# Performance work log

Hardware: AMD Instinct MI355X
Metric: run time of the kernel (lower is better)

Reference implementation:

```python
import jax, jax.numpy as jnp
import numpy as np

B, T, D, H = 8, 2048, 1024, 128  # batch, seq (== context_length), d_model, head_size


def setup_inputs() -> dict:
    key = jax.random.key(0)
    kx, kq, kk, kv = jax.random.split(key, 4)
    scale = 0.02
    return {
        "x": jax.random.normal(kx, (B, T, D), dtype=jnp.float32),
        "Wq": jax.random.normal(kq, (D, H), dtype=jnp.float32) * scale,
        "Wk": jax.random.normal(kk, (D, H), dtype=jnp.float32) * scale,
        "Wv": jax.random.normal(kv, (D, H), dtype=jnp.float32) * scale,
    }


def reference(x, Wq, Wk, Wv):
    # bias-free linear projections (torch nn.Linear(bias=False))
    q = jnp.einsum("btd,dh->bth", x, Wq)
    k = jnp.einsum("btd,dh->bth", x, Wk)
    v = jnp.einsum("btd,dh->bth", x, Wv)
    head_size = q.shape[-1]
    # scores: [B, T, T], scaled by 1/sqrt(head_size)
    scores = jnp.einsum("bqh,bkh->bqk", q, k) * (1.0 / jnp.sqrt(jnp.float32(head_size)))
    # causal mask (tril): positions k > q get -inf before softmax
    t = scores.shape[-1]
    causal = jnp.tril(jnp.ones((t, t), dtype=bool))
    scores = jnp.where(causal, scores, -jnp.inf)
    weights = jax.nn.softmax(scores, axis=-1)
    # dropout is identity in eval mode (deterministic reference)
    return jnp.einsum("bqk,bkh->bqh", weights, v)
```

## Files before the change

kernel.cpp:

```cpp
#include <hip/hip_runtime.h>
#include <hip/hip_bf16.h>
#include <stdint.h>

typedef __bf16 bf16x8 __attribute__((ext_vector_type(8)));
typedef float f32x4 __attribute__((ext_vector_type(4)));
typedef unsigned short u16;
typedef u16 u16x8 __attribute__((ext_vector_type(8)));

#define GAS __attribute__((address_space(1)))
#define LAS __attribute__((address_space(3)))

static constexpr int Tn = 2048;
static constexpr int Dn = 1024;
static constexpr int Hn = 128;

__device__ __forceinline__ u16 bf16u(float f) {
  __bf16 h = (__bf16)f;
  return __builtin_bit_cast(u16, h);
}
__device__ __forceinline__ float u16f(u16 u) {
  uint32_t t = (uint32_t)u << 16;
  return __builtin_bit_cast(float, t);
}

__device__ __forceinline__ void gl_lds16(const void* g, void* l) {
  __builtin_amdgcn_global_load_lds((GAS void*)g, (LAS void*)l, 16, 0, 0);
}

__global__ __launch_bounds__(256) void convert_w_kernel(
    const float* __restrict__ Wq, const float* __restrict__ Wk,
    const float* __restrict__ Wv, u16* __restrict__ WT) {
  const int bid = blockIdx.x;
  const int w = bid >> 7;
  const int h = bid & 127;
  const float* src = (w == 0) ? Wq : ((w == 1) ? Wk : Wv);
  const float scale = (w == 0) ? 0.08838834764831845f : 1.0f;
  const int d0 = threadIdx.x * 4;
  ushort4 v;
  v.x = bf16u(src[(size_t)(d0 + 0) * Hn + h] * scale);
  v.y = bf16u(src[(size_t)(d0 + 1) * Hn + h] * scale);
  v.z = bf16u(src[(size_t)(d0 + 2) * Hn + h] * scale);
  v.w = bf16u(src[(size_t)(d0 + 3) * Hn + h] * scale);
  *(ushort4*)(&WT[(size_t)(w * Hn + h) * Dn + d0]) = v;
}

__global__ __launch_bounds__(512, 4) void qkv_gemm_kernel(
    const float* __restrict__ x, const u16* __restrict__ WT,
    u16* __restrict__ qb, u16* __restrict__ kb, u16* __restrict__ vb) {
  __shared__ u16 As[32 * 64];
  __shared__ u16 Bs[384 * 64];
  const int m0 = blockIdx.x * 32;
  const int tid = threadIdx.x;
  const int lane = tid & 63;
  const int wid = tid >> 6;
  const int l15 = lane & 15;
  const int g = lane >> 4;
  const int g4 = g * 4;

  const f32x4 fz = {0.f, 0.f, 0.f, 0.f};
  f32x4 acc[2][3];
#pragma unroll
  for (int i = 0; i < 2; ++i)
#pragma unroll
    for (int j = 0; j < 3; ++j) acc[i][j] = fz;

  const int arow = tid >> 4;
  const int c16 = tid & 15;
  const int aslot = (c16 >> 1) ^ (arow & 7);
  const int ahalf = c16 & 1;
  const float* aptr = x + (size_t)(m0 + arow) * Dn + c16 * 4;

  float4 fa = *(const float4*)(aptr);

  for (int k0 = 0; k0 < Dn; k0 += 64) {
    {
      ushort4 pk;
      pk.x = bf16u(fa.x); pk.y = bf16u(fa.y); pk.z = bf16u(fa.z); pk.w = bf16u(fa.w);
      *(ushort4*)(&As[arow * 64 + aslot * 8 + ahalf * 4]) = pk;
    }
#pragma unroll
    for (int i = 0; i < 6; ++i) {
      const int s = i * 512 + tid;
      const int n = s >> 3;
      const int us = s & 7;
      const u16* gsrc = WT + (size_t)n * Dn + k0 + ((us ^ (n & 7)) * 8);
      gl_lds16(gsrc, &Bs[(i * 512 + wid * 64) * 8]);
    }
    __syncthreads();
    {
      const int k1 = (k0 + 64 < Dn) ? k0 + 64 : k0;
      fa = *(const float4*)(aptr + k1);
    }
#pragma unroll
    for (int kc = 0; kc < 2; ++kc) {
      bf16x8 af[2], bfr[3];
#pragma unroll
      for (int mi = 0; mi < 2; ++mi) {
        const int row = mi * 16 + l15;
        af[mi] = *(const bf16x8*)(&As[row * 64 + (((kc * 4 + g) ^ (row & 7)) * 8)]);
      }
#pragma unroll
      for (int ni = 0; ni < 3; ++ni) {
        const int n = wid * 48 + ni * 16 + l15;
        bfr[ni] = *(const bf16x8*)(&Bs[n * 64 + (((kc * 4 + g) ^ (n & 7)) * 8)]);
      }
#pragma unroll
      for (int mi = 0; mi < 2; ++mi)
#pragma unroll
        for (int ni = 0; ni < 3; ++ni)
          acc[mi][ni] = __builtin_amdgcn_mfma_f32_16x16x32_bf16(af[mi], bfr[ni], acc[mi][ni], 0, 0, 0);
    }
    __builtin_amdgcn_s_barrier();
  }
#pragma unroll
  for (int mi = 0; mi < 2; ++mi)
#pragma unroll
    for (int ni = 0; ni < 3; ++ni) {
      const int nb = wid * 48 + ni * 16;
      const int w = nb >> 7;
      u16* dst = (w == 0) ? qb : ((w == 1) ? kb : vb);
      const int h = (nb & 127) + l15;
#pragma unroll
      for (int r = 0; r < 4; ++r)
        dst[(size_t)(m0 + mi * 16 + g4 + r) * Hn + h] = bf16u(acc[mi][ni][r]);
    }
}

__global__ __launch_bounds__(256) void transpose_v_kernel(
    const u16* __restrict__ vb, u16* __restrict__ vt) {
  __shared__ u16 tile[64 * 64];
  const int bid = blockIdx.x;
  const int b = bid >> 6;
  const int rem = bid & 63;
  const int t0 = (rem >> 1) * 64, h0 = (rem & 1) * 64;
  const int tid = threadIdx.x;
  {
    const int r = tid >> 2, cq = tid & 3;
    const u16* src = vb + (size_t)(b * Tn + t0 + r) * Hn + h0 + cq * 16;
#pragma unroll
    for (int s = 0; s < 2; ++s) {
      u16x8 v = *(const u16x8*)(src + s * 8);
      const int u = cq * 2 + s;
      *(u16x8*)(&tile[r * 64 + (u ^ (r & 7)) * 8]) = v;
    }
  }
  __syncthreads();
  {
    const int hr = tid >> 2, tg = tid & 3;
    u16 outv[16];
#pragma unroll
    for (int j = 0; j < 16; ++j) {
      const int tl = tg * 16 + j;
      outv[j] = tile[tl * 64 + (((hr >> 3) ^ (tl & 7)) * 8) + (hr & 7)];
    }
    u16* dstp = vt + (size_t)(b * Hn + h0 + hr) * Tn + t0 + tg * 16;
    *(u16x8*)(dstp) = *(const u16x8*)(&outv[0]);
    *(u16x8*)(dstp + 8) = *(const u16x8*)(&outv[8]);
  }
}

__global__ __launch_bounds__(256, 2) void attention_kernel(
    const u16* __restrict__ qb, const u16* __restrict__ kb,
    const u16* __restrict__ vt, u16* __restrict__ po,
    float* __restrict__ pm, float* __restrict__ pl) {
  __shared__ u16 Ks[2][64 * 128];
  __shared__ u16 Vs[2][128 * 64];
  __shared__ u16 Pb[4][16 * 64];

  const int bid = blockIdx.x;
  const int b = bid & 7;
  const int rest = bid >> 3;
  const int s = rest & 1;
  const int kk = rest >> 1;
  const int qblk = (kk & 1) ? (kk >> 1) : (31 - (kk >> 1));
  const int qb0 = qblk * 64;

  const int tid = threadIdx.x;
  const int wid = tid >> 6;
  const int lane = tid & 63;
  const int l15 = lane & 15;
  const int g = lane >> 4;
  const int g4 = g * 4;
  const int t0w = qb0 + wid * 16;

  const u16* qB = qb + (size_t)b * Tn * Hn;
  const u16* kB = kb + (size_t)b * Tn * Hn;
  const u16* vB = vt + (size_t)b * Hn * Tn;

  bf16x8 qf[4];
#pragma unroll
  for (int kc = 0; kc < 4; ++kc)
    qf[kc] = *(const bf16x8*)(qB + (size_t)(t0w + l15) * Hn + kc * 32 + g * 8);

  const f32x4 fz = {0.f, 0.f, 0.f, 0.f};
  f32x4 o[8];
#pragma unroll
  for (int hc = 0; hc < 8; ++hc) o[hc] = fz;
  float m[4], lsum[4];
#pragma unroll
  for (int r = 0; r < 4; ++r) { m[r] = -__builtin_inff(); lsum[r] = 0.f; }

  u16* P = &Pb[wid][0];
  const int ntiles = (qblk >= s) ? ((qblk - s) >> 1) + 1 : 0;

  auto stage = [&](int buf, int kv0) {
#pragma unroll
    for (int j = 0; j < 4; ++j) {
      const int U = j * 256 + tid;
      const int row = U >> 4, us = U & 15;
      const u16* gsrc = kB + (size_t)(kv0 + row) * Hn + ((us ^ (row & 15)) * 8);
      gl_lds16(gsrc, &Ks[buf][(j * 256 + wid * 64) * 8]);
    }
#pragma unroll
    for (int j = 0; j < 4; ++j) {
      const int U = j * 256 + tid;
      const int h = U >> 3, us = U & 7;
      const u16* gsrc = vB + (size_t)h * Tn + kv0 + ((us ^ (h & 7)) * 8);
      gl_lds16(gsrc, &Vs[buf][(j * 256 + wid * 64) * 8]);
    }
  };

  if (ntiles > 0) {
    stage(0, s * 64);
    __syncthreads();
    for (int i = 0; i < ntiles; ++i) {
      const int cur = i & 1;
      if (i + 1 < ntiles) stage(cur ^ 1, (s + 2 * (i + 1)) * 64);
      const int kv0 = (s + 2 * i) * 64;
      const u16* Kl = &Ks[cur][0];
      const u16* Vl = &Vs[cur][0];

      f32x4 S[4];
#pragma unroll
      for (int cn = 0; cn < 4; ++cn) S[cn] = fz;
#pragma unroll
      for (int cn = 0; cn < 4; ++cn) {
#pragma unroll
        for (int kc = 0; kc < 4; ++kc) {
          const int row = cn * 16 + l15;
          const int unit = (kc * 4 + g) ^ (row & 15);
          const bf16x8 kf = *(const bf16x8*)(&Kl[row * 128 + unit * 8]);
          S[cn] = __builtin_amdgcn_mfma_f32_16x16x32_bf16(qf[kc], kf, S[cn], 0, 0, 0);
        }
      }
      if (kv0 + 63 > t0w) {
#pragma unroll
        for (int cn = 0; cn < 4; ++cn) {
          const int kv = kv0 + cn * 16 + l15;
#pragma unroll
          for (int r = 0; r < 4; ++r)
            if (kv > t0w + g4 + r) S[cn][r] = -__builtin_inff();
        }
      }
      float mloc[4];
#pragma unroll
      for (int r = 0; r < 4; ++r)
        mloc[r] = fmaxf(fmaxf(S[0][r], S[1][r]), fmaxf(S[2][r], S[3][r]));
#pragma unroll
      for (int st = 1; st <= 8; st <<= 1)
#pragma unroll
        for (int r = 0; r < 4; ++r)
          mloc[r] = fmaxf(mloc[r], __shfl_xor(mloc[r], st, 64));
      float sc[4], mnew[4];
#pragma unroll
      for (int r = 0; r < 4; ++r) {
        mnew[r] = fmaxf(m[r], mloc[r]);
        sc[r] = __expf(m[r] - mnew[r]);
        m[r] = mnew[r];
      }
      float psum[4] = {0.f, 0.f, 0.f, 0.f};
#pragma unroll
      for (int cn = 0; cn < 4; ++cn)
#pragma unroll
        for (int r = 0; r < 4; ++r) {
          const float p = __expf(S[cn][r] - mnew[r]);
          S[cn][r] = p;
          psum[r] += p;
        }
#pragma unroll
      for (int st = 1; st <= 8; st <<= 1)
#pragma unroll
        for (int r = 0; r < 4; ++r) psum[r] += __shfl_xor(psum[r], st, 64);
#pragma unroll
      for (int r = 0; r < 4; ++r) lsum[r] = lsum[r] * sc[r] + psum[r];
#pragma unroll
      for (int hc = 0; hc < 8; ++hc)
#pragma unroll
        for (int r = 0; r < 4; ++r) o[hc][r] *= sc[r];
      asm volatile("s_waitcnt lgkmcnt(0)" ::: "memory");
#pragma unroll
      for (int cn = 0; cn < 4; ++cn)
#pragma unroll
        for (int r = 0; r < 4; ++r) {
          const int q = g4 + r;
          const int col = cn * 16 + l15;
          P[q * 64 + (col ^ ((q & 7) << 3))] = bf16u(S[cn][r]);
        }
      asm volatile("s_waitcnt lgkmcnt(0)" ::: "memory");
      bf16x8 pf[2];
#pragma unroll
      for (int kvc = 0; kvc < 2; ++kvc)
        pf[kvc] = *(const bf16x8*)(&P[l15 * 64 + (((kvc * 32 + g * 8) ^ ((l15 & 7) << 3)))]);
#pragma unroll
      for (int hc = 0; hc < 8; ++hc) {
#pragma unroll
        for (int kvc = 0; kvc < 2; ++kvc) {
          const int h = hc * 16 + l15;
          const int unit = (kvc * 4 + g) ^ (h & 7);
          const bf16x8 vf = *(const bf16x8*)(&Vl[h * 64 + unit * 8]);
          o[hc] = __builtin_amdgcn_mfma_f32_16x16x32_bf16(pf[kvc], vf, o[hc], 0, 0, 0);
        }
      }
      __syncthreads();
    }
  }

  u16* poS = po + ((size_t)(s * 8 + b) * Tn + t0w) * Hn;
#pragma unroll
  for (int hc = 0; hc < 8; ++hc)
#pragma unroll
    for (int r = 0; r < 4; ++r)
      poS[(size_t)(g4 + r) * Hn + hc * 16 + l15] = bf16u(o[hc][r]);
  if (l15 == 0) {
#pragma unroll
    for (int r = 0; r < 4; ++r) {
      pm[(size_t)(s * 8 + b) * Tn + t0w + g4 + r] = m[r];
      pl[(size_t)(s * 8 + b) * Tn + t0w + g4 + r] = lsum[r];
    }
  }
}

__global__ __launch_bounds__(256) void merge_kernel(
    const u16* __restrict__ po, const float* __restrict__ pm,
    const float* __restrict__ pl, float* __restrict__ out) {
  const int tid = threadIdx.x;
  const int row = blockIdx.x * 8 + (tid >> 5);
  const int h0 = (tid & 31) * 4;
  const float m0 = pm[row], m1 = pm[8 * Tn + row];
  const float l0 = pl[row], l1 = pl[8 * Tn + row];
  const float M = fmaxf(m0, m1);
  const float e0 = __expf(m0 - M), e1 = __expf(m1 - M);
  const float invL = 1.0f / (e0 * l0 + e1 * l1);
  const ushort4 a = *(const ushort4*)(po + (size_t)row * Hn + h0);
  const ushort4 c = *(const ushort4*)(po + (size_t)(8 * Tn + row) * Hn + h0);
  float4 r;
  r.x = (e0 * u16f(a.x) + e1 * u16f(c.x)) * invL;
  r.y = (e0 * u16f(a.y) + e1 * u16f(c.y)) * invL;
  r.z = (e0 * u16f(a.z) + e1 * u16f(c.z)) * invL;
  r.w = (e0 * u16f(a.w) + e1 * u16f(c.w)) * invL;
  *(float4*)(out + (size_t)row * Hn + h0) = r;
}

extern "C" void kernel_launch(void* const* d_in, const int* in_sizes, int n_in,
                              void* d_out, int out_size, void* d_ws, size_t ws_size,
                              hipStream_t stream) {
  const float* x  = (const float*)d_in[0];
  const float* Wq = (const float*)d_in[1];
  const float* Wk = (const float*)d_in[2];
  const float* Wv = (const float*)d_in[3];
  float* out = (float*)d_out;
  char* ws = (char*)d_ws;
  u16* WT = (u16*)(ws);
  u16* qb = (u16*)(ws + (1u << 20));
  u16* kb = (u16*)(ws + (5u << 20));
  u16* vb = (u16*)(ws + (9u << 20));
  u16* vt = (u16*)(ws + (13u << 20));
  u16* po = (u16*)(ws + (17u << 20));
  float* pm = (float*)(ws + (25u << 20));
  float* pl = (float*)(ws + (25u << 20) + (1u << 18));

  convert_w_kernel<<<384, 256, 0, stream>>>(Wq, Wk, Wv, WT);
  qkv_gemm_kernel<<<512, 512, 0, stream>>>(x, WT, qb, kb, vb);
  transpose_v_kernel<<<512, 256, 0, stream>>>(vb, vt);
  attention_kernel<<<512, 256, 0, stream>>>(qb, kb, vt, po, pm, pl);
  merge_kernel<<<2048, 256, 0, stream>>>(po, pm, pl, out);
}
```

Measured before the change: 165.4 us.

## Fuse V transpose into QKV GEMM epilogue and double-buffer with larger M tile

The QKV projection kernel now processes 64 rows per block instead of 32, double-buffers its A and B shared-memory tiles so the next k-slice loads while the current one computes, and writes V directly in transposed layout. This removes the separate transpose kernel launch and the extra round-trip of V through global memory, and it halves redundant re-reads of the weight matrix. In exchange it doubles LDS use per block, lowers the occupancy hint from 4 to 2, and launches only 256 blocks. The transposed V stores are 4-element ushort4 writes strided by T.

```diff
diff --git a/kernel.cpp b/kernel.cpp
--- a/kernel.cpp
+++ b/kernel.cpp
@@ -44,12 +44,12 @@
   *(ushort4*)(&WT[(size_t)(w * Hn + h) * Dn + d0]) = v;
 }
 
-__global__ __launch_bounds__(512, 4) void qkv_gemm_kernel(
+__global__ __launch_bounds__(512, 2) void qkv_gemm_kernel(
     const float* __restrict__ x, const u16* __restrict__ WT,
-    u16* __restrict__ qb, u16* __restrict__ kb, u16* __restrict__ vb) {
-  __shared__ u16 As[32 * 64];
-  __shared__ u16 Bs[384 * 64];
-  const int m0 = blockIdx.x * 32;
+    u16* __restrict__ qb, u16* __restrict__ kb, u16* __restrict__ vt) {
+  __shared__ u16 As[2][64 * 64];
+  __shared__ u16 Bs[2][384 * 64];
+  const int m0 = blockIdx.x * 64;
   const int tid = threadIdx.x;
   const int lane = tid & 63;
   const int wid = tid >> 6;
@@ -58,105 +58,98 @@
   const int g4 = g * 4;
 
   const f32x4 fz = {0.f, 0.f, 0.f, 0.f};
-  f32x4 acc[2][3];
-#pragma unroll
-  for (int i = 0; i < 2; ++i)
+  f32x4 acc[4][3];
+#pragma unroll
+  for (int i = 0; i < 4; ++i)
 #pragma unroll
     for (int j = 0; j < 3; ++j) acc[i][j] = fz;
 
-  const int arow = tid >> 4;
+  const int row0 = tid >> 4;
+  const int row1 = row0 + 32;
   const int c16 = tid & 15;
-  const int aslot = (c16 >> 1) ^ (arow & 7);
+  const int slot0 = (c16 >> 1) ^ (row0 & 7);
+  const int slot1 = (c16 >> 1) ^ (row1 & 7);
   const int ahalf = c16 & 1;
-  const float* aptr = x + (size_t)(m0 + arow) * Dn + c16 * 4;
-
-  float4 fa = *(const float4*)(aptr);
-
-  for (int k0 = 0; k0 < Dn; k0 += 64) {
-    {
-      ushort4 pk;
-      pk.x = bf16u(fa.x); pk.y = bf16u(fa.y); pk.z = bf16u(fa.z); pk.w = bf16u(fa.w);
-      *(ushort4*)(&As[arow * 64 + aslot * 8 + ahalf * 4]) = pk;
-    }
+  const float* a0p = x + (size_t)(m0 + row0) * Dn + c16 * 4;
+  const float* a1p = x + (size_t)(m0 + row1) * Dn + c16 * 4;
+
+  auto stageB = [&](int buf, int k0) {
 #pragma unroll
     for (int i = 0; i < 6; ++i) {
       const int s = i * 512 + tid;
       const int n = s >> 3;
       const int us = s & 7;
       const u16* gsrc = WT + (size_t)n * Dn + k0 + ((us ^ (n & 7)) * 8);
-      gl_lds16(gsrc, &Bs[(i * 512 + wid * 64) * 8]);
-    }
+      gl_lds16(gsrc, &Bs[buf][(i * 512 + wid * 64) * 8]);
+    }
+  };
+  auto writeA = [&](int buf, float4 f0, float4 f1) {
+    ushort4 p0, p1;
+    p0.x = bf16u(f0.x); p0.y = bf16u(f0.y); p0.z = bf16u(f0.z); p0.w = bf16u(f0.w);
+    p1.x = bf16u(f1.x); p1.y = bf16u(f1.y); p1.z = bf16u(f1.z); p1.w = bf16u(f1.w);
+    *(ushort4*)(&As[buf][row0 * 64 + slot0 * 8 + ahalf * 4]) = p0;
+    *(ushort4*)(&As[buf][row1 * 64 + slot1 * 8 + ahalf * 4]) = p1;
+  };
+
+  {
+    const float4 f0 = *(const float4*)(a0p);
+    const float4 f1 = *(const float4*)(a1p);
+    writeA(0, f0, f1);
+    stageB(0, 0);
+  }
+  int cur = 0;
+  for (int k = 0; k < 16; ++k) {
     __syncthreads();
-    {
-      const int k1 = (k0 + 64 < Dn) ? k0 + 64 : k0;
-      fa = *(const float4*)(aptr + k1);
+    float4 n0, n1;
+    if (k < 15) {
+      n0 = *(const float4*)(a0p + (k + 1) * 64);
+      n1 = *(const float4*)(a1p + (k + 1) * 64);
+      stageB(cur ^ 1, (k + 1) * 64);
     }
 #pragma unroll
     for (int kc = 0; kc < 2; ++kc) {
-      bf16x8 af[2], bfr[3];
-#pragma unroll
-      for (int mi = 0; mi < 2; ++mi) {
+      bf16x8 af[4], bfr[3];
+#pragma unroll
+      for (int mi = 0; mi < 4; ++mi) {
         const int row = mi * 16 + l15;
-        af[mi] = *(const bf16x8*)(&As[row * 64 + (((kc * 4 + g) ^ (row & 7)) * 8)]);
+        af[mi] = *(const bf16x8*)(&As[cur][row * 64 + (((kc * 4 + g) ^ (row & 7)) * 8)]);
       }
 #pragma unroll
       for (int ni = 0; ni < 3; ++ni) {
         const int n = wid * 48 + ni * 16 + l15;
-        bfr[ni] = *(const bf16x8*)(&Bs[n * 64 + (((kc * 4 + g) ^ (n & 7)) * 8)]);
-      }
-#pragma unroll
-      for (int mi = 0; mi < 2; ++mi)
+        bfr[ni] = *(const bf16x8*)(&Bs[cur][n * 64 + (((kc * 4 + g) ^ (n & 7)) * 8)]);
+      }
+#pragma unroll
+      for (int mi = 0; mi < 4; ++mi)
 #pragma unroll
         for (int ni = 0; ni < 3; ++ni)
           acc[mi][ni] = __builtin_amdgcn_mfma_f32_16x16x32_bf16(af[mi], bfr[ni], acc[mi][ni], 0, 0, 0);
     }
-    __builtin_amdgcn_s_barrier();
+    if (k < 15) writeA(cur ^ 1, n0, n1);
+    cur ^= 1;
   }
 #pragma unroll
-  for (int mi = 0; mi < 2; ++mi)
+  for (int mi = 0; mi < 4; ++mi)
 #pragma unroll
     for (int ni = 0; ni < 3; ++ni) {
       const int nb = wid * 48 + ni * 16;
       const int w = nb >> 7;
-      u16* dst = (w == 0) ? qb : ((w == 1) ? kb : vb);
-      const int h = (nb & 127) + l15;
-#pragma unroll
-      for (int r = 0; r < 4; ++r)
-        dst[(size_t)(m0 + mi * 16 + g4 + r) * Hn + h] = bf16u(acc[mi][ni][r]);
-    }
-}
-
-__global__ __launch_bounds__(256) void transpose_v_kernel(
-    const u16* __restrict__ vb, u16* __restrict__ vt) {
-  __shared__ u16 tile[64 * 64];
-  const int bid = blockIdx.x;
-  const int b = bid >> 6;
-  const int rem = bid & 63;
-  const int t0 = (rem >> 1) * 64, h0 = (rem & 1) * 64;
-  const int tid = threadIdx.x;
-  {
-    const int r = tid >> 2, cq = tid & 3;
-    const u16* src = vb + (size_t)(b * Tn + t0 + r) * Hn + h0 + cq * 16;
-#pragma unroll
-    for (int s = 0; s < 2; ++s) {
-      u16x8 v = *(const u16x8*)(src + s * 8);
-      const int u = cq * 2 + s;
-      *(u16x8*)(&tile[r * 64 + (u ^ (r & 7)) * 8]) = v;
-    }
-  }
-  __syncthreads();
-  {
-    const int hr = tid >> 2, tg = tid & 3;
-    u16 outv[16];
-#pragma unroll
-    for (int j = 0; j < 16; ++j) {
-      const int tl = tg * 16 + j;
-      outv[j] = tile[tl * 64 + (((hr >> 3) ^ (tl & 7)) * 8) + (hr & 7)];
-    }
-    u16* dstp = vt + (size_t)(b * Hn + h0 + hr) * Tn + t0 + tg * 16;
-    *(u16x8*)(dstp) = *(const u16x8*)(&outv[0]);
-    *(u16x8*)(dstp + 8) = *(const u16x8*)(&outv[8]);
-  }
+      const int hcol = (nb & 127) + l15;
+      const int grow0 = m0 + mi * 16 + g4;
+      if (w == 2) {
+        const int b = grow0 >> 11;
+        const int tl = grow0 & 2047;
+        ushort4 vv;
+        vv.x = bf16u(acc[mi][ni][0]); vv.y = bf16u(acc[mi][ni][1]);
+        vv.z = bf16u(acc[mi][ni][2]); vv.w = bf16u(acc[mi][ni][3]);
+        *(ushort4*)(&vt[((size_t)(b * Hn + hcol)) * Tn + tl]) = vv;
+      } else {
+        u16* dst = (w == 0) ? qb : kb;
+#pragma unroll
+        for (int r = 0; r < 4; ++r)
+          dst[(size_t)(grow0 + r) * Hn + hcol] = bf16u(acc[mi][ni][r]);
+      }
+    }
 }
 
 __global__ __launch_bounds__(256, 2) void attention_kernel(
@@ -363,15 +356,13 @@
   u16* WT = (u16*)(ws);
   u16* qb = (u16*)(ws + (1u << 20));
   u16* kb = (u16*)(ws + (5u << 20));
-  u16* vb = (u16*)(ws + (9u << 20));
-  u16* vt = (u16*)(ws + (13u << 20));
-  u16* po = (u16*)(ws + (17u << 20));
-  float* pm = (float*)(ws + (25u << 20));
-  float* pl = (float*)(ws + (25u << 20) + (1u << 18));
+  u16* vt = (u16*)(ws + (9u << 20));
+  u16* po = (u16*)(ws + (13u << 20));
+  float* pm = (float*)(ws + (22u << 20));
+  float* pl = (float*)(ws + (22u << 20) + (1u << 18));
 
   convert_w_kernel<<<384, 256, 0, stream>>>(Wq, Wk, Wv, WT);
-  qkv_gemm_kernel<<<512, 512, 0, stream>>>(x, WT, qb, kb, vb);
-  transpose_v_kernel<<<512, 256, 0, stream>>>(vb, vt);
+  qkv_gemm_kernel<<<256, 512, 0, stream>>>(x, WT, qb, kb, vt);
   attention_kernel<<<512, 256, 0, stream>>>(qb, kb, vt, po, pm, pl);
   merge_kernel<<<2048, 256, 0, stream>>>(po, pm, pl, out);
 }
```

Result: faster. 159.5 us (-3.6%).
